# Kernel optimization log

Measured on AMD Instinct MI355X. Metric: run time of the kernel, lower is better.

Reference implementation:

```python
import jax, jax.numpy as jnp
import numpy as np

B, N, C_IN = 8, 8192, 64
M, K, RADIUS = 1024, 64, 0.2   # num_centers, num_neighbors, ball radius
LAYERS = [128, 128, 256]
EPS = 1e-5


def setup_inputs() -> dict:
    key = jax.random.key(0)
    ks = jax.random.split(key, 3 + len(LAYERS))
    feat = jax.random.normal(ks[0], (B, C_IN, N), jnp.float32)
    coords = jax.random.uniform(ks[1], (B, 3, N), jnp.float32)  # unit cube
    cond = jax.random.normal(ks[2], (B, C_IN), jnp.float32)
    params = {}
    c_prev = C_IN + 3  # include_coordinates=True
    for i, c_out in enumerate(LAYERS):
        params[f"w{i}"] = jax.random.normal(ks[3 + i], (c_out, c_prev), jnp.float32) / np.sqrt(c_prev).astype(np.float32)
        params[f"b{i}"] = jnp.zeros((c_out,), jnp.float32)
        params[f"gamma{i}"] = jnp.ones((c_out,), jnp.float32)
        params[f"beta{i}"] = jnp.zeros((c_out,), jnp.float32)
        c_prev = c_out
    return {"feat": feat, "coords": coords, "cond": cond, **params}


def fps(pts, m):
    """Furthest point sampling. pts: (B,N,3) -> (B,m) int32 indices. Starts at index 0."""
    B_, N_, _ = pts.shape

    def step(carry, _):
        dist, far = carry                                   # (B,N), (B,)
        centroid = jnp.take_along_axis(pts, far[:, None, None], axis=1)  # (B,1,3)
        d = jnp.sum((pts - centroid) ** 2, -1)              # (B,N)
        dist = jnp.minimum(dist, d)
        nxt = jnp.argmax(dist, -1).astype(jnp.int32)
        return (dist, nxt), far

    init = (jnp.full((B_, N_), 1e10, jnp.float32), jnp.zeros((B_,), jnp.int32))
    _, idx = jax.lax.scan(step, init, None, length=m)
    return idx.T                                            # (B,m)


def ball_query(pts, centers, radius, k):
    """pts (B,N,3), centers (B,M,3) -> neighbor indices (B,M,k).
    First k in-radius points (original order); empty slots repeat the first hit."""
    d2 = jnp.sum((centers[:, :, None, :] - pts[:, None, :, :]) ** 2, -1)  # (B,M,N)
    within = d2 < radius * radius
    # stable sort keys: valid points (0) first, keeping original point order
    order = jnp.argsort(jnp.where(within, 0, 1).astype(jnp.int32), axis=-1, stable=True)[..., :k]
    cnt = within.sum(-1, keepdims=True)                      # (B,M,1)
    slot = jnp.arange(k)
    return jnp.where(slot < cnt, order, order[..., :1])      # pad with first valid idx


def gather(x, idx):
    """x (B,N,D), idx (B,M,K) -> (B,M,K,D)"""
    return jax.vmap(lambda a, i: a[i])(x, idx)


def reference(feat, coords, cond,
              w0, b0, gamma0, beta0,
              w1, b1, gamma1, beta1,
              w2, b2, gamma2, beta2):
    pts = coords.transpose(0, 2, 1)                          # (B,N,3)
    cidx = fps(pts, M)                                       # (B,M)
    centers = jnp.take_along_axis(pts, cidx[..., None], axis=1)  # (B,M,3)
    nidx = ball_query(pts, centers, RADIUS, K)               # (B,M,K)
    rel = gather(pts, nidx) - centers[:, :, None, :]         # (B,M,K,3) relative coords
    nfeat = gather(feat.transpose(0, 2, 1), nidx)            # (B,M,K,C)
    x = jnp.concatenate([rel, nfeat], axis=-1)               # (B,M,K,3+C), coords first
    # Shared MLP: 1x1 conv + BatchNorm (batch stats) + ReLU per layer
    for w, b, g, be in ((w0, b0, gamma0, beta0), (w1, b1, gamma1, beta1), (w2, b2, gamma2, beta2)):
        x = jnp.einsum('bmkc,oc->bmko', x, w) + b
        mu = x.mean((0, 1, 2))
        var = x.var((0, 1, 2))
        x = (x - mu) * jax.lax.rsqrt(var + EPS) * g + be
        x = jax.nn.relu(x)
    out = x.max(axis=2).transpose(0, 2, 1)                   # max over nsample -> (B,Cout,M)
    return out, centers.transpose(0, 2, 1), cond
```

## Files before the change

### kernel.cpp

```cpp
#include <hip/hip_runtime.h>

#define NB    8
#define NPTS  8192
#define NCTR  1024
#define KNN   64
#define NGRP  8192
#define SAMP  524288
#define EPSB  1e-5f

#define OFF_CIDX 0ull
#define OFF_NIDX 32768ull
#define OFF_SS   2129920ull
#define OFF_PSUM 2134016ull
#define OFF_PSQR 4231168ull
#define OFF_GMAX 6328320ull
#define OFF_GMIN 14716928ull
#define OFF_FT   23105536ull
#define OFF_Y1   31494144ull
#define NEED_BIG 165711872ull

typedef unsigned short ushort8 __attribute__((ext_vector_type(8)));
typedef short short8v __attribute__((ext_vector_type(8)));
typedef float f32x4 __attribute__((ext_vector_type(4)));

__device__ __forceinline__ unsigned short f2b(float f) {
  unsigned int u = __builtin_bit_cast(unsigned int, f);
  u += 0x7fffu + ((u >> 16) & 1u);
  return (unsigned short)(u >> 16);
}
__device__ __forceinline__ float b2f(unsigned short s) {
  unsigned int u = ((unsigned int)s) << 16;
  return __builtin_bit_cast(float, u);
}

template <int CTRL>
__device__ __forceinline__ float dppmax(float x) {
  int m = __builtin_amdgcn_update_dpp(0, __builtin_bit_cast(int, x), CTRL, 0xf, 0xf, true);
  return fmaxf(x, __builtin_bit_cast(float, m));
}

__global__ __launch_bounds__(256) void fps_kernel(const float* __restrict__ coords,
                                                  int* __restrict__ cidx,
                                                  float* __restrict__ centers_out) {
  const int b = blockIdx.x;
  const int t = threadIdx.x;
  const int wid = t >> 6, lane = t & 63;
  __shared__ float4 sc4[NPTS];
  __shared__ unsigned long long red[2][4];
  const float* cb = coords + (size_t)b * 3 * NPTS;
  for (int i = t; i < NPTS; i += 256)
    sc4[i] = make_float4(cb[i], cb[NPTS + i], cb[2 * NPTS + i], 0.f);
  __syncthreads();
  constexpr int PT = NPTS / 256;
  float px[PT], py[PT], pz[PT], dst[PT];
#pragma unroll
  for (int i = 0; i < PT; ++i) {
    int p = t * PT + i;
    px[i] = cb[p]; py[i] = cb[NPTS + p]; pz[i] = cb[2 * NPTS + p];
    dst[i] = 1e10f;
  }
  int cur = 0;
  float4 c0 = sc4[0];
  float cx = c0.x, cy = c0.y, cz = c0.z;
  int parity = 0;
  for (int s = 0; s < NCTR; ++s) {
    if (t == 0) {
      cidx[b * NCTR + s] = cur;
      centers_out[(b * 3 + 0) * NCTR + s] = cx;
      centers_out[(b * 3 + 1) * NCTR + s] = cy;
      centers_out[(b * 3 + 2) * NCTR + s] = cz;
    }
    float bv = -1.0f; int bi = 0;
#pragma unroll
    for (int i = 0; i < PT; ++i) {
      float dx = __fsub_rn(px[i], cx);
      float dy = __fsub_rn(py[i], cy);
      float dz = __fsub_rn(pz[i], cz);
      float d2 = __fadd_rn(__fadd_rn(__fmul_rn(dx, dx), __fmul_rn(dy, dy)), __fmul_rn(dz, dz));
      float nd = fminf(dst[i], d2);
      dst[i] = nd;
      if (nd > bv) { bv = nd; bi = t * PT + i; }
    }
    float r = bv;
    r = dppmax<0x111>(r);
    r = dppmax<0x112>(r);
    r = dppmax<0x114>(r);
    r = dppmax<0x118>(r);
    r = dppmax<0x142>(r);
    r = dppmax<0x143>(r);
    float wm = __builtin_bit_cast(float,
        __builtin_amdgcn_readlane(__builtin_bit_cast(int, r), 63));
    unsigned long long mask = __ballot(bv == wm);
    int widx = __shfl(bi, (int)__builtin_ctzll(mask));
    if (lane == 0)
      red[parity][wid] =
          ((unsigned long long)__builtin_bit_cast(unsigned int, wm) << 32) |
          (unsigned long long)(~(unsigned int)widx);
    __syncthreads();
    unsigned long long best = red[parity][0];
#pragma unroll
    for (int k = 1; k < 4; ++k) {
      unsigned long long o = red[parity][k];
      best = (o > best) ? o : best;
    }
    cur = (int)(~(unsigned int)best);
    float4 cc = sc4[cur];
    cx = cc.x; cy = cc.y; cz = cc.z;
    parity ^= 1;
  }
}

__global__ __launch_bounds__(256) void featT_kernel(const float* __restrict__ feat,
                                                    unsigned short* __restrict__ fT) {
  int b  = blockIdx.y;
  int j  = blockIdx.x * 64 + (threadIdx.x & 63);
  int cg = threadIdx.x >> 6;
  ushort8 v0, v1;
#pragma unroll
  for (int cc = 0; cc < 8; ++cc)
    v0[cc] = f2b(feat[((size_t)b * 64 + cg * 16 + cc) * NPTS + j]);
#pragma unroll
  for (int cc = 0; cc < 8; ++cc)
    v1[cc] = f2b(feat[((size_t)b * 64 + cg * 16 + 8 + cc) * NPTS + j]);
  unsigned short* dst = fT + ((size_t)b * NPTS + j) * 64 + cg * 16;
  *(ushort8*)dst = v0;
  *(ushort8*)(dst + 8) = v1;
}

__global__ __launch_bounds__(256) void bq_kernel(const float* __restrict__ coords,
                                                 const int* __restrict__ cidx,
                                                 int* __restrict__ nidx) {
  const int b = blockIdx.y;
  const int w = threadIdx.x >> 6, lane = threadIdx.x & 63;
  const int m = blockIdx.x * 4 + w;
  const float* cb = coords + (size_t)b * 3 * NPTS;
  const int cen = cidx[b * NCTR + m];
  const float cx = cb[cen], cy = cb[NPTS + cen], cz = cb[2 * NPTS + cen];
  int* outp = nidx + ((size_t)b * NCTR + m) * KNN;
  const float RR = (float)(0.2 * 0.2);
  int found = 0, first = -1;
  for (int chunk = 0; chunk < NPTS / 64 && found < KNN; ++chunk) {
    int p = chunk * 64 + lane;
    float dx = __fsub_rn(cx, cb[p]);
    float dy = __fsub_rn(cy, cb[NPTS + p]);
    float dz = __fsub_rn(cz, cb[2 * NPTS + p]);
    float d2 = __fadd_rn(__fadd_rn(__fmul_rn(dx, dx), __fmul_rn(dy, dy)), __fmul_rn(dz, dz));
    bool pred = d2 < RR;
    unsigned long long mask = __ballot(pred);
    if (pred) {
      int rank = __popcll(mask & ((1ull << lane) - 1ull));
      int slot = found + rank;
      if (slot < KNN) outp[slot] = p;
    }
    if (first < 0 && mask != 0ull) first = chunk * 64 + __builtin_ctzll(mask);
    found += __popcll(mask);
  }
  if (found < KNN) {
    int f = (first < 0) ? 0 : first;
    if (lane >= found) outp[lane] = f;
  }
}

template <int NL, bool READY1, bool WRITEY1>
__global__ __launch_bounds__(256) void fused_kernel(
    const unsigned short* __restrict__ fT, const float* __restrict__ coords,
    const int* __restrict__ cidx, const int* __restrict__ nidx,
    unsigned short* __restrict__ y1, const float* __restrict__ ss,
    const float* __restrict__ w0, const float* __restrict__ b0,
    const float* __restrict__ w1, const float* __restrict__ b1,
    const float* __restrict__ w2, const float* __restrict__ b2,
    float* __restrict__ psum, float* __restrict__ psqr,
    float* __restrict__ gmax, float* __restrict__ gmin) {
  __shared__ __align__(16) unsigned short Xs[4 * 64 * 128];
  __shared__ __align__(16) unsigned short Wbuf[128 * 128];
  __shared__ float s_bias[128];
  __shared__ float s_sc0[128], s_sh0[128], s_sc1[128], s_sh1[128];
  __shared__ float s_rs[4][128], s_rq[4][128];

  const int t = threadIdx.x;
  const int wg = t >> 6, lane = t & 63;
  const int r16 = lane & 15, kg = lane >> 4;
  const int g = blockIdx.x * 4 + wg;
  const int bb_ = g >> 10;
  const int rsw = lane & 7;
  unsigned short* xrow = &Xs[(wg * 64 + lane) * 128];

  if constexpr (NL >= 2 && !READY1) {
    if (t < 128) { s_sc0[t] = ss[t]; s_sh0[t] = ss[128 + t]; }
  }
  if constexpr (NL >= 3) {
    if (t < 128) { s_sc1[t] = ss[256 + t]; s_sh1[t] = ss[384 + t]; }
  }

  auto stageW = [&](const float* w, const float* bia, bool remap0, int oh) {
    for (int e = t; e < 128 * 128; e += 256) {
      int o = e >> 7, c = e & 127;
      float v;
      if (remap0) {
        int lc = (c < 64) ? (c + 3) : ((c < 67) ? (c - 64) : -1);
        v = (lc >= 0) ? w[o * 67 + lc] : 0.f;
      } else {
        v = w[((size_t)(oh * 128 + o)) * 128 + c];
      }
      Wbuf[(o << 7) + ((((c >> 3) ^ (o & 7)) << 3) | (c & 7))] = f2b(v);
    }
    if (t < 128) s_bias[t] = bia[oh * 128 + t];
  };

  auto statsOut = [&](float (&sv8)[8], float (&sq8)[8], int coff) {
#pragma unroll
    for (int nt = 0; nt < 8; ++nt) {
      sv8[nt] += __shfl_xor(sv8[nt], 16); sv8[nt] += __shfl_xor(sv8[nt], 32);
      sq8[nt] += __shfl_xor(sq8[nt], 16); sq8[nt] += __shfl_xor(sq8[nt], 32);
    }
    if (lane < 16) {
#pragma unroll
      for (int nt = 0; nt < 8; ++nt) {
        s_rs[wg][nt * 16 + lane] = sv8[nt];
        s_rq[wg][nt * 16 + lane] = sq8[nt];
      }
    }
    __syncthreads();
    if (t < 128) {
      float sB = s_rs[0][t] + s_rs[1][t] + s_rs[2][t] + s_rs[3][t];
      float qB = s_rq[0][t] + s_rq[1][t] + s_rq[2][t] + s_rq[3][t];
      psum[(size_t)blockIdx.x * 256 + coff + t] = sB;
      psqr[(size_t)blockIdx.x * 256 + coff + t] = qB;
    }
  };

  short8v a[4][4];

  if constexpr (!READY1) {
    {
      int j = nidx[(size_t)g * KNN + lane];
      int cen = cidx[g];
      const unsigned short* fr = fT + ((size_t)bb_ * NPTS + j) * 64;
#pragma unroll
      for (int ch = 0; ch < 8; ++ch)
        *(ushort8*)(xrow + ((ch ^ rsw) << 3)) = *(const ushort8*)(fr + ch * 8);
      const float* cb = coords + (size_t)bb_ * 3 * NPTS;
      float rx = __fsub_rn(cb[j], cb[cen]);
      float ry = __fsub_rn(cb[NPTS + j], cb[NPTS + cen]);
      float rz = __fsub_rn(cb[2 * NPTS + j], cb[2 * NPTS + cen]);
      ushort8 rv = {f2b(rx), f2b(ry), f2b(rz), 0, 0, 0, 0, 0};
      *(ushort8*)(xrow + ((8 ^ rsw) << 3)) = rv;
      ushort8 zz = {0, 0, 0, 0, 0, 0, 0, 0};
#pragma unroll
      for (int ch = 9; ch < 16; ++ch)
        *(ushort8*)(xrow + ((ch ^ rsw) << 3)) = zz;
    }
    stageW(w0, b0, true, 0);
    __syncthreads();

#pragma unroll
    for (int st = 0; st < 4; ++st) {
      int row = st * 16 + r16;
#pragma unroll
      for (int ks = 0; ks < 3; ++ks)
        a[st][ks] = __builtin_bit_cast(short8v,
            *(const ushort8*)&Xs[(wg * 64 + row) * 128 + (((ks * 4 + kg) ^ (row & 7)) << 3)]);
    }
    {
      float sv8[8], sq8[8];
#pragma unroll
      for (int nt = 0; nt < 8; ++nt) { sv8[nt] = 0.f; sq8[nt] = 0.f; }
#pragma unroll
      for (int nt = 0; nt < 8; ++nt) {
        int o = nt * 16 + r16;
        short8v wb[3];
#pragma unroll
        for (int ks = 0; ks < 3; ++ks)
          wb[ks] = __builtin_bit_cast(short8v,
              *(const ushort8*)&Wbuf[(o << 7) + (((ks * 4 + kg) ^ (o & 7)) << 3)]);
        float bia = s_bias[o];
        float sc = 0.f, sh = 0.f;
        if constexpr (NL >= 2) { sc = s_sc0[o]; sh = s_sh0[o]; }
#pragma unroll
        for (int st = 0; st < 4; ++st) {
          f32x4 acc = {0.f, 0.f, 0.f, 0.f};
#pragma unroll
          for (int ks = 0; ks < 3; ++ks)
            acc = __builtin_amdgcn_mfma_f32_16x16x32_bf16(a[st][ks], wb[ks], acc, 0, 0, 0);
#pragma unroll
          for (int r = 0; r < 4; ++r) {
            float v = acc[r] + bia;
            if constexpr (NL == 1) {
              sv8[nt] += v; sq8[nt] = fmaf(v, v, sq8[nt]);
            } else {
              float x = fmaxf(fmaf(v, sc, sh), 0.f);
              int row = st * 16 + kg * 4 + r;
              Xs[(wg * 64 + row) * 128 + ((((o >> 3) ^ (row & 7)) << 3) | (o & 7))] = f2b(x);
            }
          }
        }
      }
      if constexpr (NL == 1) { statsOut(sv8, sq8, 0); return; }
    }

    if constexpr (NL >= 2) {
      __syncthreads();
      stageW(w1, b1, false, 0);
      __syncthreads();
#pragma unroll
    for (int st = 0; st < 4; ++st) {
        int row = st * 16 + r16;
#pragma unroll
        for (int ks = 0; ks < 4; ++ks)
          a[st][ks] = __builtin_bit_cast(short8v,
              *(const ushort8*)&Xs[(wg * 64 + row) * 128 + (((ks * 4 + kg) ^ (row & 7)) << 3)]);
      }
      float sv8[8], sq8[8];
#pragma unroll
      for (int nt = 0; nt < 8; ++nt) { sv8[nt] = 0.f; sq8[nt] = 0.f; }
#pragma unroll
      for (int nt = 0; nt < 8; ++nt) {
        int o = nt * 16 + r16;
        short8v wb[4];
#pragma unroll
        for (int ks = 0; ks < 4; ++ks)
          wb[ks] = __builtin_bit_cast(short8v,
              *(const ushort8*)&Wbuf[(o << 7) + (((ks * 4 + kg) ^ (o & 7)) << 3)]);
        float bia = s_bias[o];
        float sc = 0.f, sh = 0.f;
        if constexpr (NL >= 3) { sc = s_sc1[o]; sh = s_sh1[o]; }
#pragma unroll
        for (int st = 0; st < 4; ++st) {
          f32x4 acc = {0.f, 0.f, 0.f, 0.f};
#pragma unroll
          for (int ks = 0; ks < 4; ++ks)
            acc = __builtin_amdgcn_mfma_f32_16x16x32_bf16(a[st][ks], wb[ks], acc, 0, 0, 0);
#pragma unroll
          for (int r = 0; r < 4; ++r) {
            float v = acc[r] + bia;
            int row = st * 16 + kg * 4 + r;
            if constexpr (NL == 2) {
              sv8[nt] += v; sq8[nt] = fmaf(v, v, sq8[nt]);
              if constexpr (WRITEY1)
                y1[((size_t)g * 64 + row) * 128 + o] = f2b(v);
            } else {
              float x = fmaxf(fmaf(v, sc, sh), 0.f);
              Xs[(wg * 64 + row) * 128 + ((((o >> 3) ^ (row & 7)) << 3) | (o & 7))] = f2b(x);
            }
          }
        }
      }
      if constexpr (NL == 2) { statsOut(sv8, sq8, 0); return; }
    }
  } else {
    __syncthreads();
    const unsigned short* yr = y1 + ((size_t)g * 64 + lane) * 128;
#pragma unroll
    for (int ch = 0; ch < 16; ++ch) {
      ushort8 vv = *(const ushort8*)(yr + ch * 8);
      ushort8 ov;
#pragma unroll
      for (int jj = 0; jj < 8; ++jj) {
        int c = ch * 8 + jj;
        ov[jj] = f2b(fmaxf(fmaf(b2f(vv[jj]), s_sc1[c], s_sh1[c]), 0.f));
      }
      *(ushort8*)(xrow + ((ch ^ rsw) << 3)) = ov;
    }
  }

  if constexpr (NL == 3) {
#pragma unroll
    for (int st = 0; st < 4; ++st) {
      int row = st * 16 + r16;
#pragma unroll
      for (int ks = 0; ks < 4; ++ks)
        a[st][ks] = __builtin_bit_cast(short8v,
            *(const ushort8*)&Xs[(wg * 64 + row) * 128 + (((ks * 4 + kg) ^ (row & 7)) << 3)]);
    }
    for (int h = 0; h < 2; ++h) {
      __syncthreads();
      stageW(w2, b2, false, h);
      __syncthreads();
      float mx8[8], mn8[8], sv8[8], sq8[8];
#pragma unroll
      for (int nt = 0; nt < 8; ++nt) { mx8[nt] = -1e30f; mn8[nt] = 1e30f; sv8[nt] = 0.f; sq8[nt] = 0.f; }
#pragma unroll
      for (int nt = 0; nt < 8; ++nt) {
        int o = nt * 16 + r16;
        short8v wb[4];
#pragma unroll
        for (int ks = 0; ks < 4; ++ks)
          wb[ks] = __builtin_bit_cast(short8v,
              *(const ushort8*)&Wbuf[(o << 7) + (((ks * 4 + kg) ^ (o & 7)) << 3)]);
        float bia = s_bias[o];
#pragma unroll
        for (int st = 0; st < 4; ++st) {
          f32x4 acc = {0.f, 0.f, 0.f, 0.f};
#pragma unroll
          for (int ks = 0; ks < 4; ++ks)
            acc = __builtin_amdgcn_mfma_f32_16x16x32_bf16(a[st][ks], wb[ks], acc, 0, 0, 0);
#pragma unroll
          for (int r = 0; r < 4; ++r) {
            float v = acc[r] + bia;
            mx8[nt] = fmaxf(mx8[nt], v); mn8[nt] = fminf(mn8[nt], v);
            sv8[nt] += v; sq8[nt] = fmaf(v, v, sq8[nt]);
          }
        }
      }
#pragma unroll
      for (int nt = 0; nt < 8; ++nt) {
        mx8[nt] = fmaxf(mx8[nt], __shfl_xor(mx8[nt], 16));
        mx8[nt] = fmaxf(mx8[nt], __shfl_xor(mx8[nt], 32));
        mn8[nt] = fminf(mn8[nt], __shfl_xor(mn8[nt], 16));
        mn8[nt] = fminf(mn8[nt], __shfl_xor(mn8[nt], 32));
      }
      if (lane < 16) {
#pragma unroll
        for (int nt = 0; nt < 8; ++nt) {
          gmax[(size_t)g * 256 + h * 128 + nt * 16 + lane] = mx8[nt];
          gmin[(size_t)g * 256 + h * 128 + nt * 16 + lane] = mn8[nt];
        }
      }
      statsOut(sv8, sq8, h * 128);
    }
  }
}

template <int O>
__global__ __launch_bounds__(256) void ss_kernel(const float* __restrict__ psum,
                                                 const float* __restrict__ psqr,
                                                 const float* __restrict__ gamma,
                                                 const float* __restrict__ beta,
                                                 float* __restrict__ ss_out) {
  int c = blockIdx.x;
  int t = threadIdx.x;
  float s = 0.f, q = 0.f;
  for (int i = t; i < 2048; i += 256) {
    s += psum[(size_t)i * 256 + c];
    q += psqr[(size_t)i * 256 + c];
  }
  int lane = t & 63, wid = t >> 6;
#pragma unroll
  for (int off = 32; off > 0; off >>= 1) { s += __shfl_down(s, off); q += __shfl_down(q, off); }
  __shared__ float rv[4], rqv[4];
  if (lane == 0) { rv[wid] = s; rqv[wid] = q; }
  __syncthreads();
  if (t == 0) {
    s = rv[0] + rv[1] + rv[2] + rv[3];
    q = rqv[0] + rqv[1] + rqv[2] + rqv[3];
    const float inv = 1.0f / (float)SAMP;
    float mu = s * inv;
    float var = fmaxf(q * inv - mu * mu, 0.f);
    float rs = 1.0f / sqrtf(var + EPSB);
    float sc = gamma[c] * rs;
    ss_out[c] = sc;
    ss_out[O + c] = beta[c] - mu * sc;
  }
}

__global__ __launch_bounds__(256) void final_kernel(const float* __restrict__ gmax,
                                                    const float* __restrict__ gmin,
                                                    const float* __restrict__ ss2,
                                                    float* __restrict__ out) {
  int b = blockIdx.x >> 5, mt = blockIdx.x & 31;
  int t = threadIdx.x;
  __shared__ float tile[32][257];
  float sc = ss2[t], sh = ss2[256 + t];
  size_t base = ((size_t)b * 1024 + mt * 32) * 256;
#pragma unroll
  for (int r = 0; r < 32; ++r) {
    float A = fmaf(gmax[base + r * 256 + t], sc, sh);
    float C = fmaf(gmin[base + r * 256 + t], sc, sh);
    tile[r][t] = fmaxf(fmaxf(A, C), 0.f);
  }
  __syncthreads();
  for (int i = t; i < 8192; i += 256) {
    int o = i >> 5, ml = i & 31;
    out[((size_t)b * 256 + o) * 1024 + mt * 32 + ml] = tile[ml][o];
  }
}

__global__ void cond_kernel(const float* __restrict__ cond, float* __restrict__ dst) {
  dst[threadIdx.x] = cond[threadIdx.x];
}

extern "C" void kernel_launch(void* const* d_in, const int* in_sizes, int n_in,
                              void* d_out, int out_size, void* d_ws, size_t ws_size,
                              hipStream_t stream) {
  const float* feat   = (const float*)d_in[0];
  const float* coords = (const float*)d_in[1];
  const float* cond   = (const float*)d_in[2];
  const float* w0  = (const float*)d_in[3];
  const float* b0  = (const float*)d_in[4];
  const float* ga0 = (const float*)d_in[5];
  const float* be0 = (const float*)d_in[6];
  const float* w1  = (const float*)d_in[7];
  const float* b1  = (const float*)d_in[8];
  const float* ga1 = (const float*)d_in[9];
  const float* be1 = (const float*)d_in[10];
  const float* w2  = (const float*)d_in[11];
  const float* b2  = (const float*)d_in[12];
  const float* ga2 = (const float*)d_in[13];
  const float* be2 = (const float*)d_in[14];

  char* ws = (char*)d_ws;
  int* cidxp = (int*)(ws + OFF_CIDX);
  int* nidxp = (int*)(ws + OFF_NIDX);
  float* ss   = (float*)(ws + OFF_SS);
  float* psum = (float*)(ws + OFF_PSUM);
  float* psqr = (float*)(ws + OFF_PSQR);
  float* gmax = (float*)(ws + OFF_GMAX);
  float* gmin = (float*)(ws + OFF_GMIN);
  unsigned short* fT = (unsigned short*)(ws + OFF_FT);
  unsigned short* y1 = (unsigned short*)(ws + OFF_Y1);

  float* out         = (float*)d_out;
  float* centers_out = out + (size_t)8 * 256 * 1024;
  float* cond_out    = centers_out + (size_t)8 * 3 * 1024;

  const bool big = (ws_size >= NEED_BIG);

  fps_kernel<<<8, 256, 0, stream>>>(coords, cidxp, centers_out);
  featT_kernel<<<dim3(128, 8), 256, 0, stream>>>(feat, fT);
  bq_kernel<<<dim3(256, 8), 256, 0, stream>>>(coords, cidxp, nidxp);

  fused_kernel<1, false, false><<<2048, 256, 0, stream>>>(
      fT, coords, cidxp, nidxp, y1, ss, w0, b0, w1, b1, w2, b2, psum, psqr, gmax, gmin);
  ss_kernel<128><<<128, 256, 0, stream>>>(psum, psqr, ga0, be0, ss);

  if (big) {
    fused_kernel<2, false, true><<<2048, 256, 0, stream>>>(
        fT, coords, cidxp, nidxp, y1, ss, w0, b0, w1, b1, w2, b2, psum, psqr, gmax, gmin);
  } else {
    fused_kernel<2, false, false><<<2048, 256, 0, stream>>>(
        fT, coords, cidxp, nidxp, y1, ss, w0, b0, w1, b1, w2, b2, psum, psqr, gmax, gmin);
  }
  ss_kernel<128><<<128, 256, 0, stream>>>(psum, psqr, ga1, be1, ss + 256);

  if (big) {
    fused_kernel<3, true, false><<<2048, 256, 0, stream>>>(
        fT, coords, cidxp, nidxp, y1, ss, w0, b0, w1, b1, w2, b2, psum, psqr, gmax, gmin);
  } else {
    fused_kernel<3, false, false><<<2048, 256, 0, stream>>>(
        fT, coords, cidxp, nidxp, y1, ss, w0, b0, w1, b1, w2, b2, psum, psqr, gmax, gmin);
  }
  ss_kernel<256><<<256, 256, 0, stream>>>(psum, psqr, ga2, be2, ss + 512);

  final_kernel<<<256, 256, 0, stream>>>(gmax, gmin, ss + 512, out);
  cond_kernel<<<1, 512, 0, stream>>>(cond, cond_out);
}
```

Measured before the change: 1.479 ms.

## Split each group's output channels across two waves in fused MLP kernel

The fused MLP kernel grows from 256 to 512 threads per block. Each neighbourhood group is now handled by a pair of waves, each computing half of the 128 output channels (64 each), instead of one wave computing all of them. Only the first wave of each pair gathers and writes the input tile. An extra barrier is added before layer 3 so the second wave sees the staged inputs. Shared-memory use stays the same, so more waves are resident per CU to hide MFMA and LDS latency, at the cost of duplicated A-fragment loads and more barrier participants.

```diff
diff --git a/kernel.cpp b/kernel.cpp
--- a/kernel.cpp
+++ b/kernel.cpp
@@ -162,7 +162,7 @@
 }
 
 template <int NL, bool READY1, bool WRITEY1>
-__global__ __launch_bounds__(256) void fused_kernel(
+__global__ __launch_bounds__(512) void fused_kernel(
     const unsigned short* __restrict__ fT, const float* __restrict__ coords,
     const int* __restrict__ cidx, const int* __restrict__ nidx,
     unsigned short* __restrict__ y1, const float* __restrict__ ss,
@@ -175,10 +175,12 @@
   __shared__ __align__(16) unsigned short Wbuf[128 * 128];
   __shared__ float s_bias[128];
   __shared__ float s_sc0[128], s_sh0[128], s_sc1[128], s_sh1[128];
-  __shared__ float s_rs[4][128], s_rq[4][128];
+  __shared__ float s_rs[8][64], s_rq[8][64];
 
   const int t = threadIdx.x;
-  const int wg = t >> 6, lane = t & 63;
+  const int wv = t >> 6, lane = t & 63;
+  const int wg = wv >> 1;
+  const int hp = wv & 1;
   const int r16 = lane & 15, kg = lane >> 4;
   const int g = blockIdx.x * 4 + wg;
   const int bb_ = g >> 10;
@@ -193,7 +195,7 @@
   }
 
   auto stageW = [&](const float* w, const float* bia, bool remap0, int oh) {
-    for (int e = t; e < 128 * 128; e += 256) {
+    for (int e = t; e < 128 * 128; e += 512) {
       int o = e >> 7, c = e & 127;
       float v;
       if (remap0) {
@@ -207,23 +209,24 @@
     if (t < 128) s_bias[t] = bia[oh * 128 + t];
   };
 
-  auto statsOut = [&](float (&sv8)[8], float (&sq8)[8], int coff) {
-#pragma unroll
-    for (int nt = 0; nt < 8; ++nt) {
-      sv8[nt] += __shfl_xor(sv8[nt], 16); sv8[nt] += __shfl_xor(sv8[nt], 32);
-      sq8[nt] += __shfl_xor(sq8[nt], 16); sq8[nt] += __shfl_xor(sq8[nt], 32);
+  auto statsOut = [&](float (&sv4)[4], float (&sq4)[4], int coff) {
+#pragma unroll
+    for (int k = 0; k < 4; ++k) {
+      sv4[k] += __shfl_xor(sv4[k], 16); sv4[k] += __shfl_xor(sv4[k], 32);
+      sq4[k] += __shfl_xor(sq4[k], 16); sq4[k] += __shfl_xor(sq4[k], 32);
     }
     if (lane < 16) {
 #pragma unroll
-      for (int nt = 0; nt < 8; ++nt) {
-        s_rs[wg][nt * 16 + lane] = sv8[nt];
-        s_rq[wg][nt * 16 + lane] = sq8[nt];
+      for (int k = 0; k < 4; ++k) {
+        s_rs[wv][k * 16 + lane] = sv4[k];
+        s_rq[wv][k * 16 + lane] = sq4[k];
       }
     }
     __syncthreads();
     if (t < 128) {
-      float sB = s_rs[0][t] + s_rs[1][t] + s_rs[2][t] + s_rs[3][t];
-      float qB = s_rq[0][t] + s_rq[1][t] + s_rq[2][t] + s_rq[3][t];
+      int hp2 = t >> 6, cl = t & 63;
+      float sB = s_rs[0 + hp2][cl] + s_rs[2 + hp2][cl] + s_rs[4 + hp2][cl] + s_rs[6 + hp2][cl];
+      float qB = s_rq[0 + hp2][cl] + s_rq[2 + hp2][cl] + s_rq[4 + hp2][cl] + s_rq[6 + hp2][cl];
       psum[(size_t)blockIdx.x * 256 + coff + t] = sB;
       psqr[(size_t)blockIdx.x * 256 + coff + t] = qB;
     }
@@ -232,7 +235,7 @@
   short8v a[4][4];
 
   if constexpr (!READY1) {
-    {
+    if (hp == 0) {
       int j = nidx[(size_t)g * KNN + lane];
       int cen = cidx[g];
       const unsigned short* fr = fT + ((size_t)bb_ * NPTS + j) * 64;
@@ -262,12 +265,12 @@
             *(const ushort8*)&Xs[(wg * 64 + row) * 128 + (((ks * 4 + kg) ^ (row & 7)) << 3)]);
     }
     {
-      float sv8[8], sq8[8];
-#pragma unroll
-      for (int nt = 0; nt < 8; ++nt) { sv8[nt] = 0.f; sq8[nt] = 0.f; }
-#pragma unroll
-      for (int nt = 0; nt < 8; ++nt) {
-        int o = nt * 16 + r16;
+      float sv4[4], sq4[4];
+#pragma unroll
+      for (int k = 0; k < 4; ++k) { sv4[k] = 0.f; sq4[k] = 0.f; }
+#pragma unroll
+      for (int k = 0; k < 4; ++k) {
+        int o = hp * 64 + k * 16 + r16;
         short8v wb[3];
 #pragma unroll
         for (int ks = 0; ks < 3; ++ks)
@@ -286,7 +289,7 @@
           for (int r = 0; r < 4; ++r) {
             float v = acc[r] + bia;
             if constexpr (NL == 1) {
-              sv8[nt] += v; sq8[nt] = fmaf(v, v, sq8[nt]);
+              sv4[k] += v; sq4[k] = fmaf(v, v, sq4[k]);
             } else {
               float x = fmaxf(fmaf(v, sc, sh), 0.f);
               int row = st * 16 + kg * 4 + r;
@@ -295,7 +298,7 @@
           }
         }
       }
-      if constexpr (NL == 1) { statsOut(sv8, sq8, 0); return; }
+      if constexpr (NL == 1) { statsOut(sv4, sq4, 0); return; }
     }
 
     if constexpr (NL >= 2) {
@@ -303,19 +306,19 @@
       stageW(w1, b1, false, 0);
       __syncthreads();
 #pragma unroll
-    for (int st = 0; st < 4; ++st) {
+      for (int st = 0; st < 4; ++st) {
         int row = st * 16 + r16;
 #pragma unroll
         for (int ks = 0; ks < 4; ++ks)
           a[st][ks] = __builtin_bit_cast(short8v,
               *(const ushort8*)&Xs[(wg * 64 + row) * 128 + (((ks * 4 + kg) ^ (row & 7)) << 3)]);
       }
-      float sv8[8], sq8[8];
-#pragma unroll
-      for (int nt = 0; nt < 8; ++nt) { sv8[nt] = 0.f; sq8[nt] = 0.f; }
-#pragma unroll
-      for (int nt = 0; nt < 8; ++nt) {
-        int o = nt * 16 + r16;
+      float sv4[4], sq4[4];
+#pragma unroll
+      for (int k = 0; k < 4; ++k) { sv4[k] = 0.f; sq4[k] = 0.f; }
+#pragma unroll
+      for (int k = 0; k < 4; ++k) {
+        int o = hp * 64 + k * 16 + r16;
         short8v wb[4];
 #pragma unroll
         for (int ks = 0; ks < 4; ++ks)
@@ -335,7 +338,7 @@
             float v = acc[r] + bia;
             int row = st * 16 + kg * 4 + r;
             if constexpr (NL == 2) {
-              sv8[nt] += v; sq8[nt] = fmaf(v, v, sq8[nt]);
+              sv4[k] += v; sq4[k] = fmaf(v, v, sq4[k]);
               if constexpr (WRITEY1)
                 y1[((size_t)g * 64 + row) * 128 + o] = f2b(v);
             } else {
@@ -345,25 +348,28 @@
           }
         }
       }
-      if constexpr (NL == 2) { statsOut(sv8, sq8, 0); return; }
+      if constexpr (NL == 2) { statsOut(sv4, sq4, 0); return; }
     }
   } else {
     __syncthreads();
-    const unsigned short* yr = y1 + ((size_t)g * 64 + lane) * 128;
-#pragma unroll
-    for (int ch = 0; ch < 16; ++ch) {
-      ushort8 vv = *(const ushort8*)(yr + ch * 8);
-      ushort8 ov;
-#pragma unroll
-      for (int jj = 0; jj < 8; ++jj) {
-        int c = ch * 8 + jj;
-        ov[jj] = f2b(fmaxf(fmaf(b2f(vv[jj]), s_sc1[c], s_sh1[c]), 0.f));
-      }
-      *(ushort8*)(xrow + ((ch ^ rsw) << 3)) = ov;
+    if (hp == 0) {
+      const unsigned short* yr = y1 + ((size_t)g * 64 + lane) * 128;
+#pragma unroll
+      for (int ch = 0; ch < 16; ++ch) {
+        ushort8 vv = *(const ushort8*)(yr + ch * 8);
+        ushort8 ov;
+#pragma unroll
+        for (int jj = 0; jj < 8; ++jj) {
+          int c = ch * 8 + jj;
+          ov[jj] = f2b(fmaxf(fmaf(b2f(vv[jj]), s_sc1[c], s_sh1[c]), 0.f));
+        }
+        *(ushort8*)(xrow + ((ch ^ rsw) << 3)) = ov;
+      }
     }
   }
 
   if constexpr (NL == 3) {
+    __syncthreads();
 #pragma unroll
     for (int st = 0; st < 4; ++st) {
       int row = st * 16 + r16;
@@ -376,12 +382,12 @@
       __syncthreads();
       stageW(w2, b2, false, h);
       __syncthreads();
-      float mx8[8], mn8[8], sv8[8], sq8[8];
-#pragma unroll
-      for (int nt = 0; nt < 8; ++nt) { mx8[nt] = -1e30f; mn8[nt] = 1e30f; sv8[nt] = 0.f; sq8[nt] = 0.f; }
-#pragma unroll
-      for (int nt = 0; nt < 8; ++nt) {
-        int o = nt * 16 + r16;
+      float mx4[4], mn4[4], sv4[4], sq4[4];
+#pragma unroll
+      for (int k = 0; k < 4; ++k) { mx4[k] = -1e30f; mn4[k] = 1e30f; sv4[k] = 0.f; sq4[k] = 0.f; }
+#pragma unroll
+      for (int k = 0; k < 4; ++k) {
+        int o = hp * 64 + k * 16 + r16;
         short8v wb[4];
 #pragma unroll
         for (int ks = 0; ks < 4; ++ks)
@@ -397,26 +403,26 @@
 #pragma unroll
           for (int r = 0; r < 4; ++r) {
             float v = acc[r] + bia;
-            mx8[nt] = fmaxf(mx8[nt], v); mn8[nt] = fminf(mn8[nt], v);
-            sv8[nt] += v; sq8[nt] = fmaf(v, v, sq8[nt]);
+            mx4[k] = fmaxf(mx4[k], v); mn4[k] = fminf(mn4[k], v);
+            sv4[k] += v; sq4[k] = fmaf(v, v, sq4[k]);
           }
         }
       }
 #pragma unroll
-      for (int nt = 0; nt < 8; ++nt) {
-        mx8[nt] = fmaxf(mx8[nt], __shfl_xor(mx8[nt], 16));
-        mx8[nt] = fmaxf(mx8[nt], __shfl_xor(mx8[nt], 32));
-        mn8[nt] = fminf(mn8[nt], __shfl_xor(mn8[nt], 16));
-        mn8[nt] = fminf(mn8[nt], __shfl_xor(mn8[nt], 32));
+      for (int k = 0; k < 4; ++k) {
+        mx4[k] = fmaxf(mx4[k], __shfl_xor(mx4[k], 16));
+        mx4[k] = fmaxf(mx4[k], __shfl_xor(mx4[k], 32));
+        mn4[k] = fminf(mn4[k], __shfl_xor(mn4[k], 16));
+        mn4[k] = fminf(mn4[k], __shfl_xor(mn4[k], 32));
       }
       if (lane < 16) {
 #pragma unroll
-        for (int nt = 0; nt < 8; ++nt) {
-          gmax[(size_t)g * 256 + h * 128 + nt * 16 + lane] = mx8[nt];
-          gmin[(size_t)g * 256 + h * 128 + nt * 16 + lane] = mn8[nt];
+        for (int k = 0; k < 4; ++k) {
+          gmax[(size_t)g * 256 + h * 128 + hp * 64 + k * 16 + lane] = mx4[k];
+          gmin[(size_t)g * 256 + h * 128 + hp * 64 + k * 16 + lane] = mn4[k];
         }
       }
-      statsOut(sv8, sq8, h * 128);
+      statsOut(sv4, sq4, h * 128);
     }
   }
 }
@@ -519,24 +525,24 @@
   featT_kernel<<<dim3(128, 8), 256, 0, stream>>>(feat, fT);
   bq_kernel<<<dim3(256, 8), 256, 0, stream>>>(coords, cidxp, nidxp);
 
-  fused_kernel<1, false, false><<<2048, 256, 0, stream>>>(
+  fused_kernel<1, false, false><<<2048, 512, 0, stream>>>(
       fT, coords, cidxp, nidxp, y1, ss, w0, b0, w1, b1, w2, b2, psum, psqr, gmax, gmin);
   ss_kernel<128><<<128, 256, 0, stream>>>(psum, psqr, ga0, be0, ss);
 
   if (big) {
-    fused_kernel<2, false, true><<<2048, 256, 0, stream>>>(
+    fused_kernel<2, false, true><<<2048, 512, 0, stream>>>(
         fT, coords, cidxp, nidxp, y1, ss, w0, b0, w1, b1, w2, b2, psum, psqr, gmax, gmin);
   } else {
-    fused_kernel<2, false, false><<<2048, 256, 0, stream>>>(
+    fused_kernel<2, false, false><<<2048, 512, 0, stream>>>(
         fT, coords, cidxp, nidxp, y1, ss, w0, b0, w1, b1, w2, b2, psum, psqr, gmax, gmin);
   }
   ss_kernel<128><<<128, 256, 0, stream>>>(psum, psqr, ga1, be1, ss + 256);
 
   if (big) {
-    fused_kernel<3, true, false><<<2048, 256, 0, stream>>>(
+    fused_kernel<3, true, false><<<2048, 512, 0, stream>>>(
         fT, coords, cidxp, nidxp, y1, ss, w0, b0, w1, b1, w2, b2, psum, psqr, gmax, gmin);
   } else {
-    fused_kernel<3, false, false><<<2048, 256, 0, stream>>>(
+    fused_kernel<3, false, false><<<2048, 512, 0, stream>>>(
         fT, coords, cidxp, nidxp, y1, ss, w0, b0, w1, b1, w2, b2, psum, psqr, gmax, gmin);
   }
   ss_kernel<256><<<256, 256, 0, stream>>>(psum, psqr, ga2, be2, ss + 512);
```

New measurement: 1.320 ms. -10.8%, faster.
